# Optimization experiments

Measured on AMD Instinct MI355X. Metric: run time of the kernel, lower is better.

Reference implementation:

```python
import jax, jax.numpy as jnp
import numpy as np

N = 50000
E = 600000
HIDDEN = 128
HEADS = 4
HEAD_DIM = HIDDEN // HEADS
NEG_SLOPE = 0.2
LN_EPS = 1e-5


def setup_inputs() -> dict:
    key = jax.random.key(0)
    ks = jax.random.split(key, 16)
    s = 1.0 / np.sqrt(HIDDEN)
    inp = {
        "h": jax.random.normal(ks[0], (N, HIDDEN), dtype=jnp.float32),
        "src": jax.random.randint(ks[1], (E,), 0, N, dtype=jnp.int32),
        "dst": jax.random.randint(ks[2], (E,), 0, N, dtype=jnp.int32),
        # GATv2 params (share_weights=False, bias=True)
        "W_src": jax.random.normal(ks[3], (HIDDEN, HIDDEN), dtype=jnp.float32) * s,
        "b_src": jnp.zeros((HIDDEN,), dtype=jnp.float32),
        "W_dst": jax.random.normal(ks[4], (HIDDEN, HIDDEN), dtype=jnp.float32) * s,
        "b_dst": jnp.zeros((HIDDEN,), dtype=jnp.float32),
        "attn": jax.random.normal(ks[5], (HEADS, HEAD_DIM), dtype=jnp.float32) * s,
        # FFN params
        "W1": jax.random.normal(ks[6], (HIDDEN, 2 * HIDDEN), dtype=jnp.float32) * s,
        "bf1": jnp.zeros((2 * HIDDEN,), dtype=jnp.float32),
        "W2": jax.random.normal(ks[7], (2 * HIDDEN, HIDDEN), dtype=jnp.float32) * (1.0 / np.sqrt(2 * HIDDEN)),
        "bf2": jnp.zeros((HIDDEN,), dtype=jnp.float32),
        # LayerNorms
        "g1": jnp.ones((HIDDEN,), dtype=jnp.float32),
        "beta1": jnp.zeros((HIDDEN,), dtype=jnp.float32),
        "g2": jnp.ones((HIDDEN,), dtype=jnp.float32),
        "beta2": jnp.zeros((HIDDEN,), dtype=jnp.float32),
    }
    return inp


def _layernorm(x, g, b):
    mu = jnp.mean(x, axis=-1, keepdims=True)
    var = jnp.mean(jnp.square(x - mu), axis=-1, keepdims=True)
    return (x - mu) * jax.lax.rsqrt(var + LN_EPS) * g + b


def reference(h, src, dst, W_src, b_src, W_dst, b_dst, attn,
              W1, bf1, W2, bf2, g1, beta1, g2, beta2):
    # --- GATv2 attention (eval mode, dropouts are identity) ---
    fs = (h @ W_src + b_src).reshape(N, HEADS, HEAD_DIM)   # [N,H,D]
    fd = (h @ W_dst + b_dst).reshape(N, HEADS, HEAD_DIM)
    e = jax.nn.leaky_relu(fs[src] + fd[dst], NEG_SLOPE)    # [E,H,D]
    logits = jnp.einsum('ehd,hd->eh', e, attn)             # [E,H]
    # edge softmax over incoming edges of each dst node
    m = jax.ops.segment_max(logits, dst, num_segments=N)   # [N,H]
    m = jnp.where(jnp.isfinite(m), m, 0.0)                 # guard zero-in-degree
    a = jnp.exp(logits - m[dst])                           # [E,H]
    denom = jax.ops.segment_sum(a, dst, num_segments=N)    # [N,H]
    denom = jnp.where(denom == 0.0, 1.0, denom)
    alpha = a / denom[dst]                                 # [E,H]
    msg = fs[src] * alpha[:, :, None]                      # [E,H,D]
    rst = jax.ops.segment_sum(msg, dst, num_segments=N)    # [N,H,D]
    h_attn = rst.reshape(N, HIDDEN)
    # --- residual + LN, FFN + residual + LN ---
    h1 = _layernorm(h + h_attn, g1, beta1)
    ffn = jax.nn.gelu(h1 @ W1 + bf1, approximate=False) @ W2 + bf2
    out = _layernorm(h1 + ffn, g2, beta2)
    return out
```

## Files before the change

### kernel.cpp

```cpp
#include <hip/hip_runtime.h>
#include <math.h>

#define N_NODES 50000
#define N_EDGES 600000
#define HID 128
#define FFN_HID 256
#define NEG_SLOPE 0.2f
#define LN_EPS 1e-5f
#define BKT 64
#define CSTR 16

typedef unsigned short u16;
typedef unsigned int u32;
typedef __attribute__((ext_vector_type(8))) short short8;
typedef __attribute__((ext_vector_type(4))) float floatx4;

__device__ __forceinline__ u16 f2bf(float x) {
    unsigned int u = __float_as_uint(x);
    unsigned int r = u + 0x7FFFu + ((u >> 16) & 1u);
    return (u16)(r >> 16);
}
__device__ __forceinline__ float bflo(u32 u) { return __uint_as_float(u << 16); }
__device__ __forceinline__ float bfhi(u32 u) { return __uint_as_float(u & 0xffff0000u); }
__device__ __forceinline__ u32 packbf(float lo, float hi) {
    return (u32)f2bf(lo) | ((u32)f2bf(hi) << 16);
}
__device__ __forceinline__ float bf2f(u16 v) { return __uint_as_float(((u32)v) << 16); }
__device__ __forceinline__ float gelu_fast(float v) {
    float u = 1.5957691216057308f * fmaf(0.044715f * v * v, v, v);
    return v / (1.0f + __expf(-u));
}


__global__ __launch_bounds__(256) void prep_kernel(
    const float* __restrict__ Wsrc, const float* __restrict__ Wdst,
    const float* __restrict__ W1, const float* __restrict__ W2,
    u16* __restrict__ B1, u16* __restrict__ B2, u16* __restrict__ B3,
    int* __restrict__ cursor)
{
    int b = blockIdx.x;
    if (b >= 384) {
        int i = (b - 384) * 256 + threadIdx.x;
        if (i < N_NODES * CSTR) cursor[i] = 0;
        return;
    }
    int t = b * 256 + threadIdx.x;
    const float* W; u16* out; int K, Nc, noff;
    if (t < 16384)       { W = Wsrc; out = B1; K = 128; Nc = 128; noff = 0; }
    else if (t < 32768)  { W = Wdst; out = B1; K = 128; Nc = 128; noff = 128; t -= 16384; }
    else if (t < 65536)  { W = W1;   out = B2; K = 128; Nc = 256; noff = 0;   t -= 32768; }
    else if (t < 98304)  { W = W2;   out = B3; K = 256; Nc = 128; noff = 0;   t -= 65536; }
    else return;
    int n = t % Nc, k = t / Nc;
    int ng = noff + n;
    int ksteps = K >> 5;
    int frag = (ng >> 4) * ksteps + (k >> 5);
    int lane = ((k >> 3) & 3) * 16 + (ng & 15);
    int j = k & 7;
    out[((size_t)frag * 64 + lane) * 8 + j] = f2bf(W[(size_t)k * Nc + n]);
}


__global__ __launch_bounds__(256) void scatter_gemm(
    const int* __restrict__ src, const int* __restrict__ dst,
    int* __restrict__ cursor, u16* __restrict__ ebkt,
    const float* __restrict__ h, const u16* __restrict__ Bsw,
    const float* __restrict__ bsrc, const float* __restrict__ bdst,
    u16* __restrict__ fsb, u16* __restrict__ fdb)
{
    int bid = blockIdx.x;
    bool isGemm = ((bid % 3) == 0) && (bid < 3072);
    if (!isGemm) {
        int g_lt = (bid + 2) / 3; g_lt = g_lt < 1024 ? g_lt : 1024;
        int sid = bid - g_lt;
        int e = sid * 256 + threadIdx.x;
        if (e < N_EDGES) {
            int d = dst[e];
            int slot = atomicAdd(&cursor[d * CSTR], 1);
            if (slot < BKT) ebkt[(size_t)d * BKT + slot] = (u16)src[e];
        }
        return;
    }
    int gid = bid / 3;
    int tid = threadIdx.x, wave = tid >> 6, lane = tid & 63;
    int lrow = lane & 15, lq = lane >> 4;
    short8 bfrag[4][4];
    #pragma unroll
    for (int nt = 0; nt < 4; nt++)
        #pragma unroll
        for (int ks = 0; ks < 4; ks++) {
            int frag = (wave * 4 + nt) * 4 + ks;
            bfrag[nt][ks] = *(const short8*)(Bsw + ((size_t)frag * 64 + lane) * 8);
        }
    float bias[4];
    #pragma unroll
    for (int nt = 0; nt < 4; nt++) {
        int cg = wave * 64 + nt * 16 + lrow;
        bias[nt] = (cg < HID) ? bsrc[cg] : bdst[cg - HID];
    }
    for (int mb = gid; mb < N_NODES / 16; mb += 1024) {
        int m0 = mb * 16;
        const float* hrow = h + (size_t)(m0 + lrow) * HID;
        floatx4 acc[4];
        #pragma unroll
        for (int nt = 0; nt < 4; nt++) acc[nt] = {0.f, 0.f, 0.f, 0.f};
        #pragma unroll
        for (int ks = 0; ks < 4; ks++) {
            float4 va = *(const float4*)(hrow + ks * 32 + lq * 8);
            float4 vb = *(const float4*)(hrow + ks * 32 + lq * 8 + 4);
            short8 a;
            a[0] = (short)f2bf(va.x); a[1] = (short)f2bf(va.y);
            a[2] = (short)f2bf(va.z); a[3] = (short)f2bf(va.w);
            a[4] = (short)f2bf(vb.x); a[5] = (short)f2bf(vb.y);
            a[6] = (short)f2bf(vb.z); a[7] = (short)f2bf(vb.w);
            #pragma unroll
            for (int nt = 0; nt < 4; nt++)
                acc[nt] = __builtin_amdgcn_mfma_f32_16x16x32_bf16(a, bfrag[nt][ks], acc[nt], 0, 0, 0);
        }
        #pragma unroll
        for (int nt = 0; nt < 4; nt++) {
            int cg = wave * 64 + nt * 16 + lrow;
            u16* outp = (cg < HID) ? fsb : fdb;
            int c = cg & (HID - 1);
            #pragma unroll
            for (int r = 0; r < 4; r++) {
                int row = m0 + lq * 4 + r;
                outp[(size_t)row * HID + c] = f2bf(acc[nt][r] + bias[nt]);
            }
        }
    }
}


__global__ __launch_bounds__(256) void aggregate_kernel(
    const u16* __restrict__ fsb, const u16* __restrict__ fdb,
    const float* __restrict__ h, const float* __restrict__ attn,
    const int* __restrict__ cursor, const u16* __restrict__ ebkt,
    const float* __restrict__ g1, const float* __restrict__ beta1,
    u16* __restrict__ h1b)
{
    int wave = threadIdx.x >> 6, lane = threadIdx.x & 63;
    int node = blockIdx.x * 4 + wave;
    if (node >= N_NODES) return;
    int grp = lane >> 4, fl = lane & 15;
    int f = fl * 8;

    uint4 ud = *(const uint4*)&fdb[(size_t)node * HID + f];
    float fdv[8] = { bflo(ud.x), bfhi(ud.x), bflo(ud.y), bfhi(ud.y),
                     bflo(ud.z), bfhi(ud.z), bflo(ud.w), bfhi(ud.w) };
    float4 aA = *(const float4*)&attn[f];
    float4 aB = *(const float4*)&attn[f + 4];
    float c1[8] = { 0.6f * aA.x, 0.6f * aA.y, 0.6f * aA.z, 0.6f * aA.w,
                    0.6f * aB.x, 0.6f * aB.y, 0.6f * aB.z, 0.6f * aB.w };
    float c2[8] = { 0.4f * aA.x, 0.4f * aA.y, 0.4f * aA.z, 0.4f * aA.w,
                    0.4f * aB.x, 0.4f * aB.y, 0.4f * aB.z, 0.4f * aB.w };

    int cnt = cursor[node * CSTR]; cnt = cnt < BKT ? cnt : BKT;
    const u16* brow = ebkt + (size_t)node * BKT;
    float acc[8] = {0.f, 0.f, 0.f, 0.f, 0.f, 0.f, 0.f, 0.f};
    float lsum = 0.f;

    auto loadrow = [&](int e) -> uint4 {
        int s = (int)brow[e];
        return *(const uint4*)&fsb[(size_t)s * HID + f];
    };
    auto compute = [&](uint4 u) {
        float x[8] = { bflo(u.x), bfhi(u.x), bflo(u.y), bfhi(u.y),
                       bflo(u.z), bfhi(u.z), bflo(u.w), bfhi(u.w) };
        float p = 0.f;
        #pragma unroll
        for (int i = 0; i < 8; i++) {
            float ei = x[i] + fdv[i];
            p = fmaf(c1[i], ei, p);
            p = fmaf(c2[i], fabsf(ei), p);
        }
        p += __shfl_xor(p, 1); p += __shfl_xor(p, 2);
        float w = __expf(p);
        lsum += w;
        #pragma unroll
        for (int i = 0; i < 8; i++) acc[i] = fmaf(w, x[i], acc[i]);
    };

    {
        int e = grp;
        uint4 bufA, bufB;
        bool vA = (e < cnt), vB = (e + 4 < cnt);
        if (vA) bufA = loadrow(e);
        if (vB) bufB = loadrow(e + 4);
        while (vA) {
            int en = e + 8;
            uint4 bufC; bool vC = (en < cnt);
            if (vC) bufC = loadrow(en);
            compute(bufA);
            bufA = bufB; vA = vB;
            bufB = bufC; vB = vC;
            e += 4;
        }
    }

    #pragma unroll
    for (int i = 0; i < 8; i++) {
        acc[i] += __shfl_xor(acc[i], 16);
        acc[i] += __shfl_xor(acc[i], 32);
    }
    lsum += __shfl_xor(lsum, 16); lsum += __shfl_xor(lsum, 32);

    float inv = (lsum > 0.f) ? (1.0f / lsum) : 0.f;
    float4 h0 = *(const float4*)&h[(size_t)node * HID + f];
    float4 h1v = *(const float4*)&h[(size_t)node * HID + f + 4];
    float hx[8] = { h0.x, h0.y, h0.z, h0.w, h1v.x, h1v.y, h1v.z, h1v.w };
    float o[8], s1 = 0.f, s2 = 0.f;
    #pragma unroll
    for (int i = 0; i < 8; i++) {
        o[i] = hx[i] + acc[i] * inv;
        s1 += o[i]; s2 += o[i] * o[i];
    }
    s1 += __shfl_xor(s1, 1); s2 += __shfl_xor(s2, 1);
    s1 += __shfl_xor(s1, 2); s2 += __shfl_xor(s2, 2);
    s1 += __shfl_xor(s1, 4); s2 += __shfl_xor(s2, 4);
    s1 += __shfl_xor(s1, 8); s2 += __shfl_xor(s2, 8);
    float mu = s1 * (1.0f / HID);
    float var = s2 * (1.0f / HID) - mu * mu;
    float rs = rsqrtf(var + LN_EPS);
    if (grp == 0) {
        float4 gA = *(const float4*)&g1[f], gB = *(const float4*)&g1[f + 4];
        float4 bA = *(const float4*)&beta1[f], bB = *(const float4*)&beta1[f + 4];
        float q0 = (o[0] - mu) * rs * gA.x + bA.x, q1 = (o[1] - mu) * rs * gA.y + bA.y;
        float q2 = (o[2] - mu) * rs * gA.z + bA.z, q3 = (o[3] - mu) * rs * gA.w + bA.w;
        float q4 = (o[4] - mu) * rs * gB.x + bB.x, q5 = (o[5] - mu) * rs * gB.y + bB.y;
        float q6 = (o[6] - mu) * rs * gB.z + bB.z, q7 = (o[7] - mu) * rs * gB.w + bB.w;
        uint4 ob;
        ob.x = packbf(q0, q1); ob.y = packbf(q2, q3);
        ob.z = packbf(q4, q5); ob.w = packbf(q6, q7);
        *(uint4*)&h1b[(size_t)node * HID + f] = ob;
    }
}


#define TS_PAD 8

__global__ __launch_bounds__(256) void ffn_fused(
    const u16* __restrict__ h1b,
    const u16* __restrict__ B2sw, const u16* __restrict__ B3sw,
    const float* __restrict__ bf1, const float* __restrict__ bf2,
    const float* __restrict__ g2, const float* __restrict__ beta2,
    float* __restrict__ out)
{
    __shared__ u16 ts[16][FFN_HID + TS_PAD];
    __shared__ float xs[16][HID];
    int tid = threadIdx.x, wave = tid >> 6, lane = tid & 63;
    int lrow = lane & 15, lq = lane >> 4;

    short8 b1f[4][4];
    #pragma unroll
    for (int nt = 0; nt < 4; nt++)
        #pragma unroll
        for (int ks = 0; ks < 4; ks++) {
            int frag = (wave * 4 + nt) * 4 + ks;
            b1f[nt][ks] = *(const short8*)(B2sw + ((size_t)frag * 64 + lane) * 8);
        }
    short8 b2f[2][8];
    #pragma unroll
    for (int nt = 0; nt < 2; nt++)
        #pragma unroll
        for (int ks = 0; ks < 8; ks++) {
            int frag = (wave * 2 + nt) * 8 + ks;
            b2f[nt][ks] = *(const short8*)(B3sw + ((size_t)frag * 64 + lane) * 8);
        }
    float bias1[4];
    #pragma unroll
    for (int nt = 0; nt < 4; nt++) bias1[nt] = bf1[wave * 64 + nt * 16 + lrow];
    float bias2[2];
    #pragma unroll
    for (int nt = 0; nt < 2; nt++) bias2[nt] = bf2[wave * 32 + nt * 16 + lrow];

    for (int mb = blockIdx.x; mb < N_NODES / 16; mb += gridDim.x) {
        int m0 = mb * 16;
        floatx4 acc1[4];
        #pragma unroll
        for (int nt = 0; nt < 4; nt++) acc1[nt] = {0.f, 0.f, 0.f, 0.f};
        #pragma unroll
        for (int ks = 0; ks < 4; ks++) {
            short8 a = *(const short8*)(h1b + (size_t)(m0 + lrow) * HID + ks * 32 + lq * 8);
            #pragma unroll
            for (int nt = 0; nt < 4; nt++)
                acc1[nt] = __builtin_amdgcn_mfma_f32_16x16x32_bf16(a, b1f[nt][ks], acc1[nt], 0, 0, 0);
        }
        #pragma unroll
        for (int nt = 0; nt < 4; nt++) {
            int cg = wave * 64 + nt * 16 + lrow;
            #pragma unroll
            for (int r = 0; r < 4; r++) {
                float v = acc1[nt][r] + bias1[nt];
                ts[lq * 4 + r][cg] = f2bf(gelu_fast(v));
            }
        }
        __syncthreads();
        floatx4 acc2[2];
        #pragma unroll
        for (int nt = 0; nt < 2; nt++) acc2[nt] = {0.f, 0.f, 0.f, 0.f};
        #pragma unroll
        for (int ks = 0; ks < 8; ks++) {
            short8 a = *(const short8*)&ts[lrow][ks * 32 + lq * 8];
            #pragma unroll
            for (int nt = 0; nt < 2; nt++)
                acc2[nt] = __builtin_amdgcn_mfma_f32_16x16x32_bf16(a, b2f[nt][ks], acc2[nt], 0, 0, 0);
        }
        #pragma unroll
        for (int nt = 0; nt < 2; nt++) {
            int cg = wave * 32 + nt * 16 + lrow;
            #pragma unroll
            for (int r = 0; r < 4; r++) {
                int row = m0 + lq * 4 + r;
                float resid = bf2f(h1b[(size_t)row * HID + cg]);
                xs[lq * 4 + r][cg] = acc2[nt][r] + bias2[nt] + resid;
            }
        }
        __syncthreads();
        int row = tid >> 4, c0 = (tid & 15) * 8;
        float v[8];
        float s1 = 0.f, s2 = 0.f;
        #pragma unroll
        for (int i = 0; i < 8; i++) { v[i] = xs[row][c0 + i]; s1 += v[i]; s2 += v[i] * v[i]; }
        s1 += __shfl_xor(s1, 1); s2 += __shfl_xor(s2, 1);
        s1 += __shfl_xor(s1, 2); s2 += __shfl_xor(s2, 2);
        s1 += __shfl_xor(s1, 4); s2 += __shfl_xor(s2, 4);
        s1 += __shfl_xor(s1, 8); s2 += __shfl_xor(s2, 8);
        float mu = s1 * (1.0f / HID);
        float var = s2 * (1.0f / HID) - mu * mu;
        float rs = rsqrtf(var + LN_EPS);
        float o[8];
        #pragma unroll
        for (int i = 0; i < 8; i++) o[i] = (v[i] - mu) * rs * g2[c0 + i] + beta2[c0 + i];
        float* op = out + (size_t)(m0 + row) * HID + c0;
        *(float4*)(op)     = make_float4(o[0], o[1], o[2], o[3]);
        *(float4*)(op + 4) = make_float4(o[4], o[5], o[6], o[7]);
        __syncthreads();
    }
}


extern "C" void kernel_launch(void* const* d_in, const int* in_sizes, int n_in,
                              void* d_out, int out_size, void* d_ws, size_t ws_size,
                              hipStream_t stream)
{
    const float* h    = (const float*)d_in[0];
    const int*   src  = (const int*)d_in[1];
    const int*   dst  = (const int*)d_in[2];
    const float* Wsrc = (const float*)d_in[3];
    const float* bsrc = (const float*)d_in[4];
    const float* Wdst = (const float*)d_in[5];
    const float* bdst = (const float*)d_in[6];
    const float* attn = (const float*)d_in[7];
    const float* W1   = (const float*)d_in[8];
    const float* bf1  = (const float*)d_in[9];
    const float* W2   = (const float*)d_in[10];
    const float* bf2  = (const float*)d_in[11];
    const float* g1   = (const float*)d_in[12];
    const float* beta1= (const float*)d_in[13];
    const float* g2   = (const float*)d_in[14];
    const float* beta2= (const float*)d_in[15];
    float* out = (float*)d_out;

    u16* fsb = (u16*)d_ws;
    u16* fdb = fsb + (size_t)N_NODES * HID;
    u16* h1b = fdb + (size_t)N_NODES * HID;
    u16* B1 = h1b + (size_t)N_NODES * HID;
    u16* B2 = B1 + 32768;
    u16* B3 = B2 + 32768;
    int* cursor = (int*)(B3 + 32768);
    u16* ebkt   = (u16*)(cursor + (size_t)N_NODES * CSTR);

    prep_kernel<<<384 + 3125, 256, 0, stream>>>(Wsrc, Wdst, W1, W2, B1, B2, B3, cursor);
    scatter_gemm<<<3368, 256, 0, stream>>>(src, dst, cursor, ebkt,
                                           h, B1, bsrc, bdst, fsb, fdb);
    aggregate_kernel<<<(N_NODES + 3) / 4, 256, 0, stream>>>(fsb, fdb, h, attn, cursor, ebkt, g1, beta1, h1b);
    ffn_fused<<<640, 256, 0, stream>>>(h1b, B2, B3, bf1, bf2, g2, beta2, out);
}
```

Measured before the change: 221.6 us.

## Drop weight-prep kernel, load and convert weights in-kernel, vectorize edge scatter

Removes the separate prep kernel that converted and swizzled weights to bf16. The GEMM and FFN kernels now read the fp32 weights directly and convert them into MFMA fragments per block, and the cursor array is cleared with hipMemsetAsync. The edge-scatter blocks now handle four edges per thread with vector loads, and the grid is rebalanced to 1024 GEMM blocks and 586 scatter blocks. This saves one kernel launch and an intermediate buffer, at the cost of strided, uncoalesced per-block weight loads repeated across many blocks.

```diff
diff --git a/kernel.cpp b/kernel.cpp
--- a/kernel.cpp
+++ b/kernel.cpp
@@ -32,71 +32,51 @@
 }
 
 
-__global__ __launch_bounds__(256) void prep_kernel(
-    const float* __restrict__ Wsrc, const float* __restrict__ Wdst,
-    const float* __restrict__ W1, const float* __restrict__ W2,
-    u16* __restrict__ B1, u16* __restrict__ B2, u16* __restrict__ B3,
-    int* __restrict__ cursor)
-{
-    int b = blockIdx.x;
-    if (b >= 384) {
-        int i = (b - 384) * 256 + threadIdx.x;
-        if (i < N_NODES * CSTR) cursor[i] = 0;
-        return;
-    }
-    int t = b * 256 + threadIdx.x;
-    const float* W; u16* out; int K, Nc, noff;
-    if (t < 16384)       { W = Wsrc; out = B1; K = 128; Nc = 128; noff = 0; }
-    else if (t < 32768)  { W = Wdst; out = B1; K = 128; Nc = 128; noff = 128; t -= 16384; }
-    else if (t < 65536)  { W = W1;   out = B2; K = 128; Nc = 256; noff = 0;   t -= 32768; }
-    else if (t < 98304)  { W = W2;   out = B3; K = 256; Nc = 128; noff = 0;   t -= 65536; }
-    else return;
-    int n = t % Nc, k = t / Nc;
-    int ng = noff + n;
-    int ksteps = K >> 5;
-    int frag = (ng >> 4) * ksteps + (k >> 5);
-    int lane = ((k >> 3) & 3) * 16 + (ng & 15);
-    int j = k & 7;
-    out[((size_t)frag * 64 + lane) * 8 + j] = f2bf(W[(size_t)k * Nc + n]);
-}
-
-
 __global__ __launch_bounds__(256) void scatter_gemm(
     const int* __restrict__ src, const int* __restrict__ dst,
     int* __restrict__ cursor, u16* __restrict__ ebkt,
-    const float* __restrict__ h, const u16* __restrict__ Bsw,
+    const float* __restrict__ h,
+    const float* __restrict__ Wsrc, const float* __restrict__ Wdst,
     const float* __restrict__ bsrc, const float* __restrict__ bdst,
     u16* __restrict__ fsb, u16* __restrict__ fdb)
 {
     int bid = blockIdx.x;
-    bool isGemm = ((bid % 3) == 0) && (bid < 3072);
+    bool isGemm = (bid < 1536) && ((bid % 3) != 2);
     if (!isGemm) {
-        int g_lt = (bid + 2) / 3; g_lt = g_lt < 1024 ? g_lt : 1024;
-        int sid = bid - g_lt;
-        int e = sid * 256 + threadIdx.x;
-        if (e < N_EDGES) {
-            int d = dst[e];
-            int slot = atomicAdd(&cursor[d * CSTR], 1);
-            if (slot < BKT) ebkt[(size_t)d * BKT + slot] = (u16)src[e];
+        int sid = (bid < 1536) ? (bid / 3) : (512 + bid - 1536);
+        int t4 = sid * 256 + threadIdx.x;
+        if (t4 < N_EDGES / 4) {
+            uint4 d4 = *(const uint4*)&dst[t4 * 4];
+            uint4 s4 = *(const uint4*)&src[t4 * 4];
+            int slot0 = atomicAdd(&cursor[(int)d4.x * CSTR], 1);
+            int slot1 = atomicAdd(&cursor[(int)d4.y * CSTR], 1);
+            int slot2 = atomicAdd(&cursor[(int)d4.z * CSTR], 1);
+            int slot3 = atomicAdd(&cursor[(int)d4.w * CSTR], 1);
+            if (slot0 < BKT) ebkt[(size_t)d4.x * BKT + slot0] = (u16)s4.x;
+            if (slot1 < BKT) ebkt[(size_t)d4.y * BKT + slot1] = (u16)s4.y;
+            if (slot2 < BKT) ebkt[(size_t)d4.z * BKT + slot2] = (u16)s4.z;
+            if (slot3 < BKT) ebkt[(size_t)d4.w * BKT + slot3] = (u16)s4.w;
         }
         return;
     }
-    int gid = bid / 3;
+    int gid = (bid / 3) * 2 + (bid % 3);
     int tid = threadIdx.x, wave = tid >> 6, lane = tid & 63;
     int lrow = lane & 15, lq = lane >> 4;
     short8 bfrag[4][4];
-    #pragma unroll
-    for (int nt = 0; nt < 4; nt++)
-        #pragma unroll
-        for (int ks = 0; ks < 4; ks++) {
-            int frag = (wave * 4 + nt) * 4 + ks;
-            bfrag[nt][ks] = *(const short8*)(Bsw + ((size_t)frag * 64 + lane) * 8);
-        }
     float bias[4];
     #pragma unroll
     for (int nt = 0; nt < 4; nt++) {
         int cg = wave * 64 + nt * 16 + lrow;
+        const float* Wp = (cg < HID) ? (Wsrc + cg) : (Wdst + cg - HID);
         bias[nt] = (cg < HID) ? bsrc[cg] : bdst[cg - HID];
+        #pragma unroll
+        for (int ks = 0; ks < 4; ks++) {
+            short8 b;
+            #pragma unroll
+            for (int j = 0; j < 8; j++)
+                b[j] = (short)f2bf(Wp[(size_t)(ks * 32 + lq * 8 + j) * HID]);
+            bfrag[nt][ks] = b;
+        }
     }
     for (int mb = gid; mb < N_NODES / 16; mb += 1024) {
         int m0 = mb * 16;
@@ -241,7 +221,7 @@
 
 __global__ __launch_bounds__(256) void ffn_fused(
     const u16* __restrict__ h1b,
-    const u16* __restrict__ B2sw, const u16* __restrict__ B3sw,
+    const float* __restrict__ W1, const float* __restrict__ W2,
     const float* __restrict__ bf1, const float* __restrict__ bf2,
     const float* __restrict__ g2, const float* __restrict__ beta2,
     float* __restrict__ out)
@@ -253,20 +233,30 @@
 
     short8 b1f[4][4];
     #pragma unroll
-    for (int nt = 0; nt < 4; nt++)
+    for (int nt = 0; nt < 4; nt++) {
+        int cg = wave * 64 + nt * 16 + lrow;
         #pragma unroll
         for (int ks = 0; ks < 4; ks++) {
-            int frag = (wave * 4 + nt) * 4 + ks;
-            b1f[nt][ks] = *(const short8*)(B2sw + ((size_t)frag * 64 + lane) * 8);
-        }
+            short8 b;
+            #pragma unroll
+            for (int j = 0; j < 8; j++)
+                b[j] = (short)f2bf(W1[(size_t)(ks * 32 + lq * 8 + j) * FFN_HID + cg]);
+            b1f[nt][ks] = b;
+        }
+    }
     short8 b2f[2][8];
     #pragma unroll
-    for (int nt = 0; nt < 2; nt++)
+    for (int nt = 0; nt < 2; nt++) {
+        int cg = wave * 32 + nt * 16 + lrow;
         #pragma unroll
         for (int ks = 0; ks < 8; ks++) {
-            int frag = (wave * 2 + nt) * 8 + ks;
-            b2f[nt][ks] = *(const short8*)(B3sw + ((size_t)frag * 64 + lane) * 8);
-        }
+            short8 b;
+            #pragma unroll
+            for (int j = 0; j < 8; j++)
+                b[j] = (short)f2bf(W2[(size_t)(ks * 32 + lq * 8 + j) * HID + cg]);
+            b2f[nt][ks] = b;
+        }
+    }
     float bias1[4];
     #pragma unroll
     for (int nt = 0; nt < 4; nt++) bias1[nt] = bf1[wave * 64 + nt * 16 + lrow];
@@ -365,15 +355,12 @@
     u16* fsb = (u16*)d_ws;
     u16* fdb = fsb + (size_t)N_NODES * HID;
     u16* h1b = fdb + (size_t)N_NODES * HID;
-    u16* B1 = h1b + (size_t)N_NODES * HID;
-    u16* B2 = B1 + 32768;
-    u16* B3 = B2 + 32768;
-    int* cursor = (int*)(B3 + 32768);
+    int* cursor = (int*)(h1b + (size_t)N_NODES * HID);
     u16* ebkt   = (u16*)(cursor + (size_t)N_NODES * CSTR);
 
-    prep_kernel<<<384 + 3125, 256, 0, stream>>>(Wsrc, Wdst, W1, W2, B1, B2, B3, cursor);
-    scatter_gemm<<<3368, 256, 0, stream>>>(src, dst, cursor, ebkt,
-                                           h, B1, bsrc, bdst, fsb, fdb);
+    hipMemsetAsync(cursor, 0, (size_t)N_NODES * CSTR * sizeof(int), stream);
+    scatter_gemm<<<1610, 256, 0, stream>>>(src, dst, cursor, ebkt,
+                                           h, Wsrc, Wdst, bsrc, bdst, fsb, fdb);
     aggregate_kernel<<<(N_NODES + 3) / 4, 256, 0, stream>>>(fsb, fdb, h, attn, cursor, ebkt, g1, beta1, h1b);
-    ffn_fused<<<640, 256, 0, stream>>>(h1b, B2, B3, bf1, bf2, g2, beta2, out);
-}
+    ffn_fused<<<640, 256, 0, stream>>>(h1b, W1, W2, bf1, bf2, g2, beta2, out);
+}
```

Result: no change. 221.0 us (-0.2%).
